# Performance work log

Measured on AMD Instinct MI355X. Metric: run time of the kernel, lower is better.

The kernel has to match this reference:

```python
import jax, jax.numpy as jnp
import numpy as np

D_IN = 1024
D_OUT = 1024
N = 4096


def setup_inputs() -> dict:
    key = jax.random.key(0)
    kx, kq, kk, kv = jax.random.split(key, 4)
    x = jax.random.normal(kx, (N, D_IN), dtype=jnp.float32)
    # weights stored as [d_in, d_out] so that x @ W == torch Linear(x)
    s = 1.0 / np.sqrt(D_IN)
    W_q = jax.random.uniform(kq, (D_IN, D_OUT), jnp.float32, -s, s)
    W_k = jax.random.uniform(kk, (D_IN, D_OUT), jnp.float32, -s, s)
    W_v = jax.random.uniform(kv, (D_IN, D_OUT), jnp.float32, -s, s)
    return {"x": x, "W_q": W_q, "W_k": W_k, "W_v": W_v}


def reference(x, W_q, W_k, W_v):
    # x: [N, d_in]; projections -> [N, d_out]
    q = x @ W_q
    k = x @ W_k
    v = x @ W_v
    scale = 1.0 / jnp.sqrt(jnp.asarray(k.shape[-1], dtype=q.dtype))
    scores = (q @ k.T) * scale            # [N, N]
    weights = jax.nn.softmax(scores, axis=-1)
    return weights @ v                     # [N, d_out]
```

## Files before the change

### kernel.cpp

```cpp
#include <hip/hip_runtime.h>
#include <math.h>

typedef _Float16 f16;
typedef __attribute__((ext_vector_type(8))) _Float16 f16x8;
typedef __attribute__((ext_vector_type(4))) _Float16 f16x4;
typedef __attribute__((ext_vector_type(4))) float f32x4;

#define NSEQ 4096
#define DIN 1024
#define DOUT 1024

__device__ __forceinline__ void load16(const void* g, void* l) {
    __builtin_amdgcn_global_load_lds(
        (const __attribute__((address_space(1))) unsigned int*)g,
        (__attribute__((address_space(3))) unsigned int*)l, 16, 0, 0);
}

template <typename OutT, int EPI>
__global__ __launch_bounds__(256, 2)
void gemm_bt(const f16* __restrict__ A, const f16* __restrict__ B,
             OutT* __restrict__ c0, OutT* __restrict__ c1,
             OutT* __restrict__ c2, OutT* __restrict__ c3,
             int M, int N, int K, int lda, int ldb, int ldc, float scale,
             long aStrideZ, long bStrideZ,
             f16* __restrict__ TC, int tz, int ldt, float* __restrict__ Sums)
{
    const int z = blockIdx.z;
    A += (long)z * aStrideZ;
    B += (long)z * bStrideZ;
    OutT* C = z == 0 ? c0 : (z == 1 ? c1 : (z == 2 ? c2 : c3));
    __shared__ f16 As[2 * 256 * 32];
    __shared__ f16 Bs[2 * 128 * 32];

    const int gx = gridDim.x;
    const int nwg = gx * gridDim.y;
    const int bid = blockIdx.y * gx + blockIdx.x;
    int bx, by;
    if (gx >= 8 && nwg >= 256) {
        int xcd = bid & 7, s = bid >> 3;
        int px = s & 7, rest = s >> 3;
        int py = rest & 3, chunk = rest >> 2;
        int pg = xcd + (chunk << 3);
        int pcols = gx >> 3;
        int lp = 31 - __clz(pcols);
        bx = ((pg & (pcols - 1)) << 3) + px;
        by = ((pg >> lp) << 2) + py;
    } else {
        int nb = (bid & 7) * (nwg >> 3) + (bid >> 3);
        bx = nb % gx; by = nb / gx;
    }

    const int t    = threadIdx.x;
    const int lane = t & 63;
    const int wave = t >> 6;
    const int wm   = (wave >> 1) * 128;
    const int wn   = (wave & 1) * 64;
    const int tile_m = by * 256;
    const int tile_n = bx * 128;
    const int quad = lane >> 4;
    const int l16  = lane & 15;
    const int srow = t >> 2;
    const int scol = (((t & 3) + srow + (srow >> 2)) & 3) * 8;
    const int qx8 = ((quad - (l16 + (l16 >> 2))) & 3) * 8;

    f32x4 acc[8][4];
#pragma unroll
    for (int i = 0; i < 8; i++)
#pragma unroll
        for (int j = 0; j < 4; j++)
            acc[i][j] = (f32x4){0.f, 0.f, 0.f, 0.f};

    const f16* Ab = A + (long)(tile_m + srow) * lda + scol;
    const f16* Bb = B + (long)(tile_n + srow) * ldb + scol;
    const long a64 = (long)64 * lda, b64 = (long)64 * ldb;
    f16* Asd = As + t * 8;
    f16* Bsd = Bs + t * 8;

    for (int k0 = 0; k0 < K; k0 += 64) {
        load16(Ab + k0,                Asd);
        load16(Ab + a64 + k0,          Asd + 2048);
        load16(Ab + 2 * a64 + k0,      Asd + 4096);
        load16(Ab + 3 * a64 + k0,      Asd + 6144);
        load16(Ab + k0 + 32,           Asd + 8192);
        load16(Ab + a64 + k0 + 32,     Asd + 8192 + 2048);
        load16(Ab + 2 * a64 + k0 + 32, Asd + 8192 + 4096);
        load16(Ab + 3 * a64 + k0 + 32, Asd + 8192 + 6144);
        load16(Bb + k0,                Bsd);
        load16(Bb + b64 + k0,          Bsd + 2048);
        load16(Bb + k0 + 32,           Bsd + 4096);
        load16(Bb + b64 + k0 + 32,     Bsd + 4096 + 2048);
        __syncthreads();
#pragma unroll
        for (int p = 0; p < 2; p++) {
            f16x8 a[8], b[4];
#pragma unroll
            for (int i = 0; i < 8; i++)
                a[i] = *(const f16x8*)(As + p * 8192 + (wm + i * 16 + l16) * 32 + qx8);
#pragma unroll
            for (int j = 0; j < 4; j++)
                b[j] = *(const f16x8*)(Bs + p * 4096 + (wn + j * 16 + l16) * 32 + qx8);
#pragma unroll
            for (int i = 0; i < 8; i++)
#pragma unroll
                for (int j = 0; j < 4; j++)
                    acc[i][j] = __builtin_amdgcn_mfma_f32_16x16x32_f16(
                        a[i], b[j], acc[i][j], 0, 0, 0);
        }
        __syncthreads();
    }
    if (EPI == 1) {
        if (z == tz) {
#pragma unroll
            for (int i = 0; i < 8; i++)
#pragma unroll
                for (int j = 0; j < 4; j++) {
                    f16x4 o;
#pragma unroll
                    for (int r = 0; r < 4; r++) o[r] = (f16)(acc[i][j][r] * scale);
                    int row0 = tile_m + wm + i * 16 + quad * 4;
                    int col  = tile_n + wn + j * 16 + l16;
                    *(f16x4*)(TC + (long)col * ldt + row0) = o;
                }
        } else {
#pragma unroll
            for (int i = 0; i < 8; i++)
#pragma unroll
                for (int j = 0; j < 4; j++)
#pragma unroll
                    for (int r = 0; r < 4; r++) {
                        int row = tile_m + wm + i * 16 + quad * 4 + r;
                        int col = tile_n + wn + j * 16 + l16;
                        C[(long)row * ldc + col] = (OutT)(acc[i][j][r] * scale);
                    }
        }
    } else if (EPI == 2) {
        const int bxs = bx * 2 + (wn >> 6);
#pragma unroll
        for (int i = 0; i < 8; i++) {
            float rs[4] = {0.f, 0.f, 0.f, 0.f};
#pragma unroll
            for (int j = 0; j < 4; j++)
#pragma unroll
                for (int r = 0; r < 4; r++) {
                    float e = __expf(acc[i][j][r] * scale);
                    int row = tile_m + wm + i * 16 + quad * 4 + r;
                    int col = tile_n + wn + j * 16 + l16;
                    C[(long)row * ldc + col] = (OutT)e;
                    rs[r] += e;
                }
#pragma unroll
            for (int msk = 1; msk < 16; msk <<= 1)
#pragma unroll
                for (int r = 0; r < 4; r++)
                    rs[r] += __shfl_xor(rs[r], msk, 64);
            if (l16 == 0)
#pragma unroll
                for (int r = 0; r < 4; r++) {
                    int row = tile_m + wm + i * 16 + quad * 4 + r;
                    Sums[(long)row * 64 + bxs] = rs[r];
                }
        }
    } else {
#pragma unroll
        for (int i = 0; i < 8; i++)
#pragma unroll
            for (int j = 0; j < 4; j++)
#pragma unroll
                for (int r = 0; r < 4; r++) {
                    int row = tile_m + wm + i * 16 + quad * 4 + r;
                    int col = tile_n + wn + j * 16 + l16;
                    C[(long)row * ldc + col] = (OutT)(acc[i][j][r] * scale);
                }
    }
}

__global__ void prep(const float* __restrict__ x,
                     const float* __restrict__ W0, const float* __restrict__ W1,
                     const float* __restrict__ W2,
                     f16* __restrict__ xb, f16* __restrict__ Wt) {
    if (blockIdx.z == 3) {
        long base = ((long)(blockIdx.y * 16 + blockIdx.x) * 256 + threadIdx.x) * 4;
#pragma unroll
        for (int it = 0; it < 16; it++) {
            long i = base + (long)it * (256 * 256 * 4);
            f32x4 v = *(const f32x4*)(x + i);
            f16x4 o;
            o.x = (f16)v.x; o.y = (f16)v.y; o.z = (f16)v.z; o.w = (f16)v.w;
            *(f16x4*)(xb + i) = o;
        }
        return;
    }
    __shared__ f16 tile[64][65];
    const float* W = blockIdx.z == 0 ? W0 : (blockIdx.z == 1 ? W1 : W2);
    f16* O = Wt + (long)blockIdx.z * DIN * DOUT;
    int r0 = blockIdx.y * 64;
    int c0 = blockIdx.x * 64;
    int tx = threadIdx.x & 63, ty = threadIdx.x >> 6;
#pragma unroll
    for (int i = 0; i < 16; i++)
        tile[ty + i * 4][tx] = (f16)W[(long)(r0 + ty + i * 4) * DOUT + c0 + tx];
    __syncthreads();
#pragma unroll
    for (int i = 0; i < 16; i++)
        O[(long)(c0 + ty + i * 4) * DIN + r0 + tx] = tile[tx][ty + i * 4];
}

__global__ __launch_bounds__(256)
void reduce_norm(const f16* __restrict__ p0, const f16* __restrict__ p1,
                 const f16* __restrict__ p2, const f16* __restrict__ p3,
                 const float* __restrict__ sums, float* __restrict__ out) {
    const int row = blockIdx.x;
    const int lane = threadIdx.x & 63;
    float s = sums[(long)row * 64 + lane];
#pragma unroll
    for (int msk = 1; msk < 64; msk <<= 1) s += __shfl_xor(s, msk, 64);
    const float inv = 1.f / s;
    long i = (long)row * 1024 + threadIdx.x * 4;
    f16x4 a = *(const f16x4*)(p0 + i);
    f16x4 b = *(const f16x4*)(p1 + i);
    f16x4 c = *(const f16x4*)(p2 + i);
    f16x4 d = *(const f16x4*)(p3 + i);
    f32x4 o;
    o.x = (((float)a.x + (float)b.x) + ((float)c.x + (float)d.x)) * inv;
    o.y = (((float)a.y + (float)b.y) + ((float)c.y + (float)d.y)) * inv;
    o.z = (((float)a.z + (float)b.z) + ((float)c.z + (float)d.z)) * inv;
    o.w = (((float)a.w + (float)b.w) + ((float)c.w + (float)d.w)) * inv;
    *(f32x4*)(out + i) = o;
}

extern "C" void kernel_launch(void* const* d_in, const int* in_sizes, int n_in,
                              void* d_out, int out_size, void* d_ws, size_t ws_size,
                              hipStream_t stream) {
    const float* x  = (const float*)d_in[0];
    const float* Wq = (const float*)d_in[1];
    const float* Wk = (const float*)d_in[2];
    const float* Wv = (const float*)d_in[3];
    float* out = (float*)d_out;
    char* ws = (char*)d_ws;
    const size_t MB = 1ull << 20;
    f16* xb  = (f16*)(ws);
    f16* Wt  = (f16*)(ws + 8 * MB);
    f16* Qb  = (f16*)(ws + 14 * MB);
    f16* Kb  = (f16*)(ws + 22 * MB);
    f16* Vt  = (f16*)(ws + 30 * MB);
    f16* S   = (f16*)(ws + 38 * MB);
    f16* scr0 = (f16*)(ws + 70 * MB);
    f16* scr1 = (f16*)(ws + 78 * MB);
    f16* scr2 = (f16*)(ws + 86 * MB);
    f16* scr3 = (f16*)(ws + 94 * MB);
    float* Sums = (float*)(ws);

    prep<<<dim3(16, 16, 4), 256, 0, stream>>>(x, Wq, Wk, Wv, xb, Wt);
    gemm_bt<f16, 1><<<dim3(8, 16, 3), 256, 0, stream>>>(
        xb, Wt, Qb, Kb, Qb, Qb, NSEQ, DOUT, DIN, DIN, DIN, DOUT, 1.0f,
        0, (long)DIN * DOUT, Vt, 2, NSEQ, nullptr);
    gemm_bt<f16, 2><<<dim3(32, 16, 1), 256, 0, stream>>>(
        Qb, Kb, S, S, S, S, NSEQ, NSEQ, DIN, DIN, DIN, NSEQ, 0.03125f,
        0, 0, nullptr, -1, 0, Sums);
    gemm_bt<f16, 0><<<dim3(8, 16, 4), 256, 0, stream>>>(
        S, Vt, scr0, scr1, scr2, scr3, NSEQ, DOUT, 1024, NSEQ, NSEQ, DOUT, 1.0f,
        1024, 1024, nullptr, -1, 0, nullptr);
    reduce_norm<<<4096, 256, 0, stream>>>(scr0, scr1, scr2, scr3, Sums, out);
}
```

Measured before the change: 204.9 us.

## Split QKV projection into 128x128-tile GEMM and stagger workgroup start with sleeps

```diff
diff --git a/kernel.cpp b/kernel.cpp
--- a/kernel.cpp
+++ b/kernel.cpp
@@ -16,14 +16,139 @@
         (__attribute__((address_space(3))) unsigned int*)l, 16, 0, 0);
 }
 
+
 template <typename OutT, int EPI>
 __global__ __launch_bounds__(256, 2)
-void gemm_bt(const f16* __restrict__ A, const f16* __restrict__ B,
-             OutT* __restrict__ c0, OutT* __restrict__ c1,
-             OutT* __restrict__ c2, OutT* __restrict__ c3,
-             int M, int N, int K, int lda, int ldb, int ldc, float scale,
-             long aStrideZ, long bStrideZ,
-             f16* __restrict__ TC, int tz, int ldt, float* __restrict__ Sums)
+void gemm_q(const f16* __restrict__ A, const f16* __restrict__ B,
+            OutT* __restrict__ c0, OutT* __restrict__ c1,
+            OutT* __restrict__ c2, OutT* __restrict__ c3,
+            int M, int N, int K, int lda, int ldb, int ldc, float scale,
+            long aStrideZ, long bStrideZ,
+            f16* __restrict__ TC, int tz, int ldt)
+{
+    const int z = blockIdx.z;
+    A += (long)z * aStrideZ;
+    B += (long)z * bStrideZ;
+    OutT* C = z == 0 ? c0 : (z == 1 ? c1 : (z == 2 ? c2 : c3));
+    __shared__ f16 As[2 * 128 * 32];
+    __shared__ f16 Bs[2 * 128 * 32];
+
+    int gx = gridDim.x;
+    int bid = blockIdx.y * gx + blockIdx.x;
+    {
+        int fid = blockIdx.z * (gx * gridDim.y) + bid;
+        int ph = (fid >> 8) & 3;
+        if (ph & 1) __builtin_amdgcn_s_sleep(12);
+        if (ph & 2) { __builtin_amdgcn_s_sleep(12); __builtin_amdgcn_s_sleep(12); }
+    }
+    int xcd = bid & 7, s = bid >> 3;
+    int px = s & 7, rest = s >> 3;
+    int py = rest & 3, chunk = rest >> 2;
+    int pg = xcd + (chunk << 3);
+    int pcols = gx >> 3;
+    int lp = 31 - __clz(pcols);
+    int bx = ((pg & (pcols - 1)) << 3) + px;
+    int by = ((pg >> lp) << 2) + py;
+
+    const int t    = threadIdx.x;
+    const int lane = t & 63;
+    const int wave = t >> 6;
+    const int wm   = (wave >> 1) * 64;
+    const int wn   = (wave & 1) * 64;
+    const int tile_m = by * 128;
+    const int tile_n = bx * 128;
+    const int quad = lane >> 4;
+    const int l16  = lane & 15;
+    const int srow = t >> 2;
+    const int scol = (((t & 3) + srow + (srow >> 2)) & 3) * 8;
+    const int qx8 = ((quad - (l16 + (l16 >> 2))) & 3) * 8;
+
+    f32x4 acc[4][4];
+#pragma unroll
+    for (int i = 0; i < 4; i++)
+#pragma unroll
+        for (int j = 0; j < 4; j++)
+            acc[i][j] = (f32x4){0.f, 0.f, 0.f, 0.f};
+
+    const f16* Ab = A + (long)(tile_m + srow) * lda + scol;
+    const f16* Bb = B + (long)(tile_n + srow) * ldb + scol;
+    f16* Asd = As + t * 8;
+    f16* Bsd = Bs + t * 8;
+
+    for (int k0 = 0; k0 < K; k0 += 64) {
+        load16(Ab + k0, Asd);
+        load16(Ab + (long)64 * lda + k0, Asd + 2048);
+        load16(Ab + k0 + 32, Asd + 4096);
+        load16(Ab + (long)64 * lda + k0 + 32, Asd + 4096 + 2048);
+        load16(Bb + k0, Bsd);
+        load16(Bb + (long)64 * ldb + k0, Bsd + 2048);
+        load16(Bb + k0 + 32, Bsd + 4096);
+        load16(Bb + (long)64 * ldb + k0 + 32, Bsd + 4096 + 2048);
+        __syncthreads();
+#pragma unroll
+        for (int p = 0; p < 2; p++) {
+            f16x8 a[4], b[4];
+#pragma unroll
+            for (int i = 0; i < 4; i++)
+                a[i] = *(const f16x8*)(As + p * 4096 + (wm + i * 16 + l16) * 32 + qx8);
+#pragma unroll
+            for (int j = 0; j < 4; j++)
+                b[j] = *(const f16x8*)(Bs + p * 4096 + (wn + j * 16 + l16) * 32 + qx8);
+#pragma unroll
+            for (int i = 0; i < 4; i++)
+#pragma unroll
+                for (int j = 0; j < 4; j++)
+                    acc[i][j] = __builtin_amdgcn_mfma_f32_16x16x32_f16(
+                        a[i], b[j], acc[i][j], 0, 0, 0);
+        }
+        __syncthreads();
+    }
+    if (EPI == 1) {
+        if (z == tz) {
+#pragma unroll
+            for (int i = 0; i < 4; i++)
+#pragma unroll
+                for (int j = 0; j < 4; j++) {
+                    f16x4 o;
+#pragma unroll
+                    for (int r = 0; r < 4; r++) o[r] = (f16)(acc[i][j][r] * scale);
+                    int row0 = tile_m + wm + i * 16 + quad * 4;
+                    int col  = tile_n + wn + j * 16 + l16;
+                    *(f16x4*)(TC + (long)col * ldt + row0) = o;
+                }
+        } else {
+#pragma unroll
+            for (int i = 0; i < 4; i++)
+#pragma unroll
+                for (int j = 0; j < 4; j++)
+#pragma unroll
+                    for (int r = 0; r < 4; r++) {
+                        int row = tile_m + wm + i * 16 + quad * 4 + r;
+                        int col = tile_n + wn + j * 16 + l16;
+                        C[(long)row * ldc + col] = (OutT)(acc[i][j][r] * scale);
+                    }
+        }
+    } else {
+#pragma unroll
+        for (int i = 0; i < 4; i++)
+#pragma unroll
+            for (int j = 0; j < 4; j++)
+#pragma unroll
+                for (int r = 0; r < 4; r++) {
+                    int row = tile_m + wm + i * 16 + quad * 4 + r;
+                    int col = tile_n + wn + j * 16 + l16;
+                    C[(long)row * ldc + col] = (OutT)(acc[i][j][r] * scale);
+                }
+    }
+}
+
+template <typename OutT, int EPI>
+__global__ __launch_bounds__(256, 2)
+void gemm_w(const f16* __restrict__ A, const f16* __restrict__ B,
+            OutT* __restrict__ c0, OutT* __restrict__ c1,
+            OutT* __restrict__ c2, OutT* __restrict__ c3,
+            int M, int N, int K, int lda, int ldb, int ldc, float scale,
+            long aStrideZ, long bStrideZ, float* __restrict__ Sums)
 {
     const int z = blockIdx.z;
     A += (long)z * aStrideZ;
@@ -35,6 +160,12 @@
     const int gx = gridDim.x;
     const int nwg = gx * gridDim.y;
     const int bid = blockIdx.y * gx + blockIdx.x;
+    {
+        int fid = blockIdx.z * nwg + bid;
+        if ((fid >> 8) & 1) {
+            __builtin_amdgcn_s_sleep(13); __builtin_amdgcn_s_sleep(13);
+        }
+    }
     int bx, by;
     if (gx >= 8 && nwg >= 256) {
         int xcd = bid & 7, s = bid >> 3;
@@ -108,32 +239,7 @@
         }
         __syncthreads();
     }
-    if (EPI == 1) {
-        if (z == tz) {
-#pragma unroll
-            for (int i = 0; i < 8; i++)
-#pragma unroll
-                for (int j = 0; j < 4; j++) {
-                    f16x4 o;
-#pragma unroll
-                    for (int r = 0; r < 4; r++) o[r] = (f16)(acc[i][j][r] * scale);
-                    int row0 = tile_m + wm + i * 16 + quad * 4;
-                    int col  = tile_n + wn + j * 16 + l16;
-                    *(f16x4*)(TC + (long)col * ldt + row0) = o;
-                }
-        } else {
-#pragma unroll
-            for (int i = 0; i < 8; i++)
-#pragma unroll
-                for (int j = 0; j < 4; j++)
-#pragma unroll
-                    for (int r = 0; r < 4; r++) {
-                        int row = tile_m + wm + i * 16 + quad * 4 + r;
-                        int col = tile_n + wn + j * 16 + l16;
-                        C[(long)row * ldc + col] = (OutT)(acc[i][j][r] * scale);
-                    }
-        }
-    } else if (EPI == 2) {
+    if (EPI == 2) {
         const int bxs = bx * 2 + (wn >> 6);
 #pragma unroll
         for (int i = 0; i < 8; i++) {
@@ -251,14 +357,14 @@
     float* Sums = (float*)(ws);
 
     prep<<<dim3(16, 16, 4), 256, 0, stream>>>(x, Wq, Wk, Wv, xb, Wt);
-    gemm_bt<f16, 1><<<dim3(8, 16, 3), 256, 0, stream>>>(
+    gemm_q<f16, 1><<<dim3(8, 32, 3), 256, 0, stream>>>(
         xb, Wt, Qb, Kb, Qb, Qb, NSEQ, DOUT, DIN, DIN, DIN, DOUT, 1.0f,
-        0, (long)DIN * DOUT, Vt, 2, NSEQ, nullptr);
-    gemm_bt<f16, 2><<<dim3(32, 16, 1), 256, 0, stream>>>(
+        0, (long)DIN * DOUT, Vt, 2, NSEQ);
+    gemm_w<f16, 2><<<dim3(32, 16, 1), 256, 0, stream>>>(
         Qb, Kb, S, S, S, S, NSEQ, NSEQ, DIN, DIN, DIN, NSEQ, 0.03125f,
-        0, 0, nullptr, -1, 0, Sums);
-    gemm_bt<f16, 0><<<dim3(8, 16, 4), 256, 0, stream>>>(
+        0, 0, Sums);
+    gemm_w<f16, 0><<<dim3(8, 16, 4), 256, 0, stream>>>(
         S, Vt, scr0, scr1, scr2, scr3, NSEQ, DOUT, 1024, NSEQ, NSEQ, DOUT, 1.0f,
-        1024, 1024, nullptr, -1, 0, nullptr);
+        1024, 1024, nullptr);
     reduce_norm<<<4096, 256, 0, stream>>>(scr0, scr1, scr2, scr3, Sums, out);
 }
```

Measured after the change: 193.3 us. -5.7%, faster.
